# Kernel optimization log

Hardware: AMD Instinct MI355X
Metric: run time of the kernel (lower is better)

## Reference

```python
import jax, jax.numpy as jnp
import numpy as np

B, N, C = 32, 2248, 1024
D = 128            # bottleneck (down_size)
P = 200            # num_prompt_tokens
SCALE = D ** (-0.5)


def setup_inputs() -> dict:
    key = jax.random.key(0)
    k = jax.random.split(key, 5)
    return {
        "x": jax.random.normal(k[0], (B, N, C), dtype=jnp.float32),
        "W_down": jax.random.normal(k[1], (C, D), dtype=jnp.float32) * (C ** -0.5),
        "b_down": jax.random.normal(k[2], (D,), dtype=jnp.float32) * 0.01,
        "W_up": jax.random.normal(k[3], (D, C), dtype=jnp.float32) * (D ** -0.5),
        "b_up": jax.random.normal(k[4], (C,), dtype=jnp.float32) * 0.01,
        "gate": jnp.ones((), dtype=jnp.float32),
    }


def reference(x, W_down, b_down, W_up, b_up, gate):
    # down-projection + exact GELU (torch nn.GELU default is erf-based)
    down = jax.nn.gelu(jnp.einsum('bnc,cd->bnd', x, W_down) + b_down,
                       approximate=False)                      # [B, N, D]
    prompt_down = down[:, :P, :]                               # [B, P, D]
    token_down = down[:, P:, :]                                # [B, N-P, D]
    # prompt-token cross attention
    attn = jax.nn.softmax(
        jnp.einsum('bpd,btd->bpt', prompt_down, token_down) * SCALE, axis=-1)
    prompt_out = jnp.einsum('bpt,btd->bpd', attn, token_down)  # [B, P, D]
    combined = jnp.concatenate([prompt_out, token_down], axis=1)  # [B, N, D]
    up = jnp.einsum('bnd,dc->bnc', combined, W_up) + b_up      # [B, N, C]
    return gate * up
```

## Files before the change

kernel.cpp:

```cpp
#include <hip/hip_runtime.h>
#include <hip/hip_bf16.h>
#include <math.h>

#define B_   32
#define N_   2248
#define C_   1024
#define D_   128
#define P_   200
#define T_   2048
#define M_   (B_ * N_)
#define SCALE_ 0.08838834764831845f

typedef __bf16 bf16;
typedef __bf16 bf16x8 __attribute__((ext_vector_type(8)));
typedef __bf16 bf16x4 __attribute__((ext_vector_type(4)));
typedef float  f32x4  __attribute__((ext_vector_type(4)));
typedef unsigned int u32x4 __attribute__((ext_vector_type(4)));

#define VT_COL(dd, t) ((((((t) >> 3) ^ (((dd) >> 3) & 7)) << 3)) | ((t) & 7))

__device__ __forceinline__ void gl_lds16(const void* g, void* l) {
    __builtin_amdgcn_global_load_lds(
        (const __attribute__((address_space(1))) unsigned int*)g,
        (__attribute__((address_space(3))) unsigned int*)l,
        16, 0, 0);
}

__global__ void k_prep(const float* __restrict__ Wd, const float* __restrict__ Wu,
                       bf16* __restrict__ WtD, bf16* __restrict__ WtU) {
    int i = blockIdx.x * 256 + threadIdx.x;
    if (i >= 131072) return;
    int d = i >> 10, k = i & 1023;
    WtD[i] = (bf16)Wd[k * 128 + d];
    int c = i >> 7, e = i & 127;
    WtU[i] = (bf16)Wu[e * 1024 + c];
}

__launch_bounds__(256, 3)
__global__ void k_down(const float* __restrict__ x, const bf16* __restrict__ WtD,
                       const float* __restrict__ bd, bf16* __restrict__ down) {
    __shared__ __align__(16) char ring[3][16384];
    const int tid = threadIdx.x;
    const int lane = tid & 63, w = tid >> 6;
    const int wm = w >> 1, wn = w & 1;
    const int li = lane & 15, lg = lane >> 4;
    const int m0 = blockIdx.x * 64;

    const int cA0 = w * 2, cA1 = w * 2 + 1;
    const int ar0 = cA0 * 8 + (lane >> 3);
    const int ar1 = cA1 * 8 + (lane >> 3);
    const float* asrc0 = x + (size_t)(m0 + ar0) * C_ + ((((lane & 7) ^ (ar0 & 7)) * 16) >> 2);
    const float* asrc1 = x + (size_t)(m0 + ar1) * C_ + ((((lane & 7) ^ (ar1 & 7)) * 16) >> 2);
    const int br0 = cA0 * 16 + (lane >> 2);
    const int br1 = cA1 * 16 + (lane >> 2);
    const bf16* bsrc0 = WtD + (size_t)br0 * C_ + (((lane & 3) ^ (br0 & 3)) * 8);
    const bf16* bsrc1 = WtD + (size_t)br1 * C_ + (((lane & 3) ^ (br1 & 3)) * 8);

#define STAGE_(t_, s_) do {                                              \
        gl_lds16(asrc0 + (t_) * 32, ring[s_] + cA0 * 1024);              \
        gl_lds16(asrc1 + (t_) * 32, ring[s_] + cA1 * 1024);              \
        gl_lds16(bsrc0 + (t_) * 32, ring[s_] + 8192 + cA0 * 1024);       \
        gl_lds16(bsrc1 + (t_) * 32, ring[s_] + 8192 + cA1 * 1024);       \
    } while (0)

    f32x4 acc[2][4];
    const f32x4 zero = {0.f, 0.f, 0.f, 0.f};
#pragma unroll
    for (int i = 0; i < 2; i++)
#pragma unroll
        for (int j = 0; j < 4; j++) acc[i][j] = zero;

    STAGE_(0, 0);
    STAGE_(1, 1);

    for (int t = 0; t < 32; t++) {
        if (t < 31) { asm volatile("s_waitcnt vmcnt(4)" ::: "memory"); }
        else        { asm volatile("s_waitcnt vmcnt(0)" ::: "memory"); }
        __builtin_amdgcn_sched_barrier(0);
        __builtin_amdgcn_s_barrier();
        __builtin_amdgcn_sched_barrier(0);
        if (t + 2 < 32) {
            int s = (t + 2) % 3;
            STAGE_(t + 2, s);
        }
        const char* sa = ring[t % 3];
        const char* sb = sa + 8192;
        bf16x8 af[2];
#pragma unroll
        for (int f = 0; f < 2; f++) {
            int row = wm * 32 + f * 16 + li;
            const char* rb = sa + row * 128;
            int p0 = (2 * lg) ^ (row & 7), p1 = (2 * lg + 1) ^ (row & 7);
            f32x4 a0 = *(const f32x4*)(rb + p0 * 16);
            f32x4 a1 = *(const f32x4*)(rb + p1 * 16);
            bf16x8 o;
            o[0] = (bf16)a0[0]; o[1] = (bf16)a0[1]; o[2] = (bf16)a0[2]; o[3] = (bf16)a0[3];
            o[4] = (bf16)a1[0]; o[5] = (bf16)a1[1]; o[6] = (bf16)a1[2]; o[7] = (bf16)a1[3];
            af[f] = o;
        }
        bf16x8 bfr[4];
#pragma unroll
        for (int f = 0; f < 4; f++) {
            int row = wn * 64 + f * 16 + li;
            bfr[f] = *(const bf16x8*)(sb + row * 64 + ((lg ^ (row & 3)) * 16));
        }
#pragma unroll
        for (int fm = 0; fm < 2; fm++)
#pragma unroll
            for (int fn = 0; fn < 4; fn++)
                acc[fm][fn] = __builtin_amdgcn_mfma_f32_16x16x32_bf16(
                    af[fm], bfr[fn], acc[fm][fn], 0, 0, 0);
    }
#undef STAGE_

#pragma unroll
    for (int fn = 0; fn < 4; fn++) {
        int col = wn * 64 + fn * 16 + li;
        float bias = bd[col];
#pragma unroll
        for (int fm = 0; fm < 2; fm++) {
            int rb = m0 + wm * 32 + fm * 16 + lg * 4;
#pragma unroll
            for (int r = 0; r < 4; r++) {
                float v = acc[fm][fn][r] + bias;
                float g = 0.5f * v * (1.0f + erff(v * 0.70710678118654752f));
                down[(size_t)(rb + r) * D_ + col] = (bf16)g;
            }
        }
    }
}

__launch_bounds__(256, 3)
__global__ void k_fused(const bf16* __restrict__ down, bf16* __restrict__ pout,
                        const bf16* __restrict__ WtU, const float* __restrict__ bu,
                        const float* __restrict__ gate, float* __restrict__ out) {
    __shared__ bf16 Ks[64][136];
    __shared__ bf16 Vt[128][72];
    __shared__ bf16 Ps[4][16][72];
    const int tid = threadIdx.x;
    const int lane = tid & 63, w = tid >> 6;
    const int li = lane & 15, lg = lane >> 4;

    if (blockIdx.x < 128) {
        const int b  = blockIdx.x >> 2;
        const int qt = blockIdx.x & 3;
        const size_t base = (size_t)b * N_ * D_;

        bf16x8 qf[4];
#pragma unroll
        for (int kk = 0; kk < 4; kk++)
            qf[kk] = *(const bf16x8*)(down + base +
                        (size_t)(qt * 64 + w * 16 + li) * D_ + kk * 32 + lg * 8);

        float m_run[4], l_run[4];
        f32x4 acc[8];
        const f32x4 zero = {0.f, 0.f, 0.f, 0.f};
#pragma unroll
        for (int r = 0; r < 4; r++) { m_run[r] = -3.0e38f; l_run[r] = 0.f; }
#pragma unroll
        for (int fn = 0; fn < 8; fn++) acc[fn] = zero;

        for (int tt = 0; tt < 32; tt++) {
            __syncthreads();
#pragma unroll
            for (int it = 0; it < 4; it++) {
                int ch = tid + it * 256;
                int r = ch >> 4, c8 = (ch & 15) * 8;
                u32x4 v = *(const u32x4*)(down + base +
                              (size_t)(P_ + tt * 64 + r) * D_ + c8);
                *(u32x4*)&Ks[r][c8] = v;
                bf16 tmp[8];
                *(u32x4*)tmp = v;
#pragma unroll
                for (int j = 0; j < 8; j++) Vt[c8 + j][VT_COL(c8 + j, r)] = tmp[j];
            }
            __syncthreads();
            f32x4 s[4];
#pragma unroll
            for (int fn = 0; fn < 4; fn++) {
                s[fn] = zero;
#pragma unroll
                for (int kk = 0; kk < 4; kk++) {
                    bf16x8 kf = *(const bf16x8*)&Ks[fn * 16 + li][kk * 32 + lg * 8];
                    s[fn] = __builtin_amdgcn_mfma_f32_16x16x32_bf16(qf[kk], kf, s[fn], 0, 0, 0);
                }
                s[fn] *= SCALE_;
            }
#pragma unroll
            for (int r = 0; r < 4; r++) {
                float tmax = fmaxf(fmaxf(s[0][r], s[1][r]), fmaxf(s[2][r], s[3][r]));
#pragma unroll
                for (int off = 1; off < 16; off <<= 1)
                    tmax = fmaxf(tmax, __shfl_xor(tmax, off, 64));
                float mnew = fmaxf(m_run[r], tmax);
                float corr = __expf(m_run[r] - mnew);
                m_run[r] = mnew;
                float psum = 0.f;
#pragma unroll
                for (int fn = 0; fn < 4; fn++) {
                    float p = __expf(s[fn][r] - mnew);
                    psum += p;
                    Ps[w][lg * 4 + r][fn * 16 + li] = (bf16)p;
                }
#pragma unroll
                for (int off = 1; off < 16; off <<= 1)
                    psum += __shfl_xor(psum, off, 64);
                l_run[r] = l_run[r] * corr + psum;
#pragma unroll
                for (int fn = 0; fn < 8; fn++) acc[fn][r] *= corr;
            }
#pragma unroll
            for (int kk = 0; kk < 2; kk++) {
                bf16x8 pf = *(const bf16x8*)&Ps[w][li][kk * 32 + lg * 8];
#pragma unroll
                for (int fn = 0; fn < 8; fn++) {
                    int d = fn * 16 + li;
                    bf16x8 vf = *(const bf16x8*)&Vt[d][VT_COL(d, kk * 32 + lg * 8)];
                    acc[fn] = __builtin_amdgcn_mfma_f32_16x16x32_bf16(pf, vf, acc[fn], 0, 0, 0);
                }
            }
        }
#pragma unroll
        for (int r = 0; r < 4; r++) {
            int q = qt * 64 + w * 16 + lg * 4 + r;
            if (q < P_) {
                float inv = 1.0f / l_run[r];
#pragma unroll
                for (int fn = 0; fn < 8; fn++)
                    pout[(size_t)(b * P_ + q) * D_ + fn * 16 + li] = (bf16)(acc[fn][r] * inv);
            }
        }
    } else {
        const int wm = w >> 1, wn = w & 1;
        int bidu = blockIdx.x - 128;
        int wg = (bidu & 7) * 512 + (bidu >> 3);
        const int b  = wg >> 7;
        const int rt = (wg >> 3) & 15;
        const int nt = wg & 7;
        const size_t m0 = (size_t)b * N_ + P_ + rt * 128;
        const int n0 = nt * 128;

        const bf16* Bp = WtU + (size_t)(n0 + wn * 64 + li) * D_ + lg * 8;

        f32x4 acc[4][4];
        const f32x4 zero = {0.f, 0.f, 0.f, 0.f};
#pragma unroll
        for (int i = 0; i < 4; i++)
#pragma unroll
            for (int j = 0; j < 4; j++) acc[i][j] = zero;

#pragma unroll
        for (int kk = 0; kk < 4; kk++) {
            bf16x8 af[4], bf_[4];
#pragma unroll
            for (int f = 0; f < 4; f++) {
                af[f]  = *(const bf16x8*)(down + (m0 + wm * 64 + f * 16 + li) * D_ + kk * 32 + lg * 8);
                bf_[f] = *(const bf16x8*)(Bp + (size_t)(f * 16) * D_ + kk * 32);
            }
#pragma unroll
            for (int fm = 0; fm < 4; fm++)
#pragma unroll
                for (int fn = 0; fn < 4; fn++)
                    acc[fm][fn] = __builtin_amdgcn_mfma_f32_16x16x32_bf16(
                        af[fm], bf_[fn], acc[fm][fn], 0, 0, 0);
        }

        float g = gate[0];
#pragma unroll
        for (int fn = 0; fn < 4; fn++) {
            int c = n0 + wn * 64 + fn * 16 + li;
            float bias = bu[c];
#pragma unroll
            for (int fm = 0; fm < 4; fm++) {
                size_t rb = m0 + wm * 64 + fm * 16 + lg * 4;
#pragma unroll
                for (int r = 0; r < 4; r++)
                    out[(rb + r) * C_ + c] = g * (acc[fm][fn][r] + bias);
            }
        }
    }
}

__launch_bounds__(256, 3)
__global__ void k_up_prompt(const bf16* __restrict__ pout, const bf16* __restrict__ WtU,
                            const float* __restrict__ bu, const float* __restrict__ gate,
                            float* __restrict__ out) {
    const int tid = threadIdx.x;
    const int lane = tid & 63, wid = tid >> 6;
    const int wm = wid >> 1, wn = wid & 1;
    const int li = lane & 15, lg = lane >> 4;
    const int b  = blockIdx.x >> 4;
    const int pt = (blockIdx.x >> 3) & 1;
    const int nt = blockIdx.x & 7;
    const int n0 = nt * 128;

    const bf16* rp[4];
#pragma unroll
    for (int f = 0; f < 4; f++) {
        int n = pt * 128 + wm * 64 + f * 16 + li;
        int nc = n < P_ ? n : P_ - 1;
        rp[f] = pout + (size_t)(b * P_ + nc) * D_ + lg * 8;
    }
    const bf16* Bp = WtU + (size_t)(n0 + wn * 64 + li) * D_ + lg * 8;

    f32x4 acc[4][4];
    const f32x4 zero = {0.f, 0.f, 0.f, 0.f};
#pragma unroll
    for (int i = 0; i < 4; i++)
#pragma unroll
        for (int j = 0; j < 4; j++) acc[i][j] = zero;

#pragma unroll
    for (int kk = 0; kk < 4; kk++) {
        bf16x8 af[4], bf_[4];
#pragma unroll
        for (int f = 0; f < 4; f++) {
            af[f]  = *(const bf16x8*)(rp[f] + kk * 32);
            bf_[f] = *(const bf16x8*)(Bp + (size_t)(f * 16) * D_ + kk * 32);
        }
#pragma unroll
        for (int fm = 0; fm < 4; fm++)
#pragma unroll
            for (int fn = 0; fn < 4; fn++)
                acc[fm][fn] = __builtin_amdgcn_mfma_f32_16x16x32_bf16(
                    af[fm], bf_[fn], acc[fm][fn], 0, 0, 0);
    }

    float g = gate[0];
#pragma unroll
    for (int fn = 0; fn < 4; fn++) {
        int c = n0 + wn * 64 + fn * 16 + li;
        float bias = bu[c];
#pragma unroll
        for (int fm = 0; fm < 4; fm++) {
            int nr = pt * 128 + wm * 64 + fm * 16 + lg * 4;
#pragma unroll
            for (int r = 0; r < 4; r++) {
                if (nr + r < P_)
                    out[((size_t)b * N_ + nr + r) * C_ + c] = g * (acc[fm][fn][r] + bias);
            }
        }
    }
}

extern "C" void kernel_launch(void* const* d_in, const int* in_sizes, int n_in,
                              void* d_out, int out_size, void* d_ws, size_t ws_size,
                              hipStream_t stream) {
    const float* x    = (const float*)d_in[0];
    const float* Wd   = (const float*)d_in[1];
    const float* bd   = (const float*)d_in[2];
    const float* Wu   = (const float*)d_in[3];
    const float* bu   = (const float*)d_in[4];
    const float* gate = (const float*)d_in[5];
    float* out = (float*)d_out;

    char* w = (char*)d_ws;
    bf16* down = (bf16*)w;
    bf16* pout = (bf16*)(w + 18415616);
    bf16* WtD  = (bf16*)(w + 20054016);
    bf16* WtU  = (bf16*)(w + 20316160);

    k_prep<<<512, 256, 0, stream>>>(Wd, Wu, WtD, WtU);
    k_down<<<M_ / 64, 256, 0, stream>>>(x, WtD, bd, down);
    k_fused<<<128 + 4096, 256, 0, stream>>>(down, pout, WtU, bu, gate, out);
    k_up_prompt<<<512, 256, 0, stream>>>(pout, WtU, bu, gate, out);
}
```

Before: 271.1 us.

## Split prompt attention over four token chunks with a separate combine kernel

The attention part of the fused kernel moves from 128 blocks that each walk all 2048 tokens to 512 blocks that each handle a quarter of the tokens. Each block writes unnormalized partial outputs plus its running max and sum, and a new combine kernel merges them with log-sum-exp rescaling into the bf16 prompt output. The goal is to cut the long serial tail of the attention blocks, which otherwise run far longer than the up-projection tiles sharing the grid. The cost is an extra kernel launch and roughly 16 MB of fp32 partial-result traffic.

```diff
diff --git a/kernel.cpp b/kernel.cpp
--- a/kernel.cpp
+++ b/kernel.cpp
@@ -131,7 +131,8 @@
 }
 
 __launch_bounds__(256, 3)
-__global__ void k_fused(const bf16* __restrict__ down, bf16* __restrict__ pout,
+__global__ void k_fused(const bf16* __restrict__ down, float* __restrict__ Opart,
+                        float* __restrict__ Mpart, float* __restrict__ Lpart,
                         const bf16* __restrict__ WtU, const float* __restrict__ bu,
                         const float* __restrict__ gate, float* __restrict__ out) {
     __shared__ bf16 Ks[64][136];
@@ -141,10 +142,14 @@
     const int lane = tid & 63, w = tid >> 6;
     const int li = lane & 15, lg = lane >> 4;
 
-    if (blockIdx.x < 128) {
-        const int b  = blockIdx.x >> 2;
-        const int qt = blockIdx.x & 3;
+    if (blockIdx.x < 512) {
+        const int bid = blockIdx.x;
+        const int wg = (bid & 7) * 64 + (bid >> 3);
+        const int b  = wg >> 4;
+        const int qt = (wg >> 2) & 3;
+        const int th = wg & 3;
         const size_t base = (size_t)b * N_ * D_;
+        const int tbase = P_ + th * 512;
 
         bf16x8 qf[4];
 #pragma unroll
@@ -160,14 +165,14 @@
 #pragma unroll
         for (int fn = 0; fn < 8; fn++) acc[fn] = zero;
 
-        for (int tt = 0; tt < 32; tt++) {
+        for (int tt = 0; tt < 8; tt++) {
             __syncthreads();
 #pragma unroll
             for (int it = 0; it < 4; it++) {
                 int ch = tid + it * 256;
                 int r = ch >> 4, c8 = (ch & 15) * 8;
                 u32x4 v = *(const u32x4*)(down + base +
-                              (size_t)(P_ + tt * 64 + r) * D_ + c8);
+                              (size_t)(tbase + tt * 64 + r) * D_ + c8);
                 *(u32x4*)&Ks[r][c8] = v;
                 bf16 tmp[8];
                 *(u32x4*)tmp = v;
@@ -223,16 +228,18 @@
 #pragma unroll
         for (int r = 0; r < 4; r++) {
             int q = qt * 64 + w * 16 + lg * 4 + r;
-            if (q < P_) {
-                float inv = 1.0f / l_run[r];
-#pragma unroll
-                for (int fn = 0; fn < 8; fn++)
-                    pout[(size_t)(b * P_ + q) * D_ + fn * 16 + li] = (bf16)(acc[fn][r] * inv);
+            size_t ro = ((size_t)(b * 4 + th) * 256 + q) * 128;
+#pragma unroll
+            for (int fn = 0; fn < 8; fn++)
+                Opart[ro + fn * 16 + li] = acc[fn][r];
+            if (li == 0) {
+                Mpart[(b * 4 + th) * 256 + q] = m_run[r];
+                Lpart[(b * 4 + th) * 256 + q] = l_run[r];
             }
         }
     } else {
         const int wm = w >> 1, wn = w & 1;
-        int bidu = blockIdx.x - 128;
+        int bidu = blockIdx.x - 512;
         int wg = (bidu & 7) * 512 + (bidu >> 3);
         const int b  = wg >> 7;
         const int rt = (wg >> 3) & 15;
@@ -279,6 +286,40 @@
             }
         }
     }
+}
+
+__global__ void k_comb(const float* __restrict__ Opart, const float* __restrict__ Mpart,
+                       const float* __restrict__ Lpart, bf16* __restrict__ pout) {
+    int gid = blockIdx.x * 256 + threadIdx.x;
+    if (gid >= (B_ * P_ * D_) / 4) return;
+    int e = gid * 4;
+    int row = e >> 7;
+    int col = e & 127;
+    int b = row / P_;
+    int q = row - b * P_;
+    float mm[4], ll[4];
+    float m = -3.0e38f;
+#pragma unroll
+    for (int t = 0; t < 4; t++) {
+        mm[t] = Mpart[(b * 4 + t) * 256 + q];
+        ll[t] = Lpart[(b * 4 + t) * 256 + q];
+        m = fmaxf(m, mm[t]);
+    }
+    float a[4], lsum = 0.f;
+#pragma unroll
+    for (int t = 0; t < 4; t++) { a[t] = __expf(mm[t] - m); lsum += ll[t] * a[t]; }
+    float inv = 1.0f / lsum;
+    f32x4 o = {0.f, 0.f, 0.f, 0.f};
+#pragma unroll
+    for (int t = 0; t < 4; t++) {
+        f32x4 ot = *(const f32x4*)&Opart[((size_t)(b * 4 + t) * 256 + q) * 128 + col];
+#pragma unroll
+        for (int j = 0; j < 4; j++) o[j] += ot[j] * a[t];
+    }
+    bf16x4 ob;
+#pragma unroll
+    for (int j = 0; j < 4; j++) ob[j] = (bf16)(o[j] * inv);
+    *(bf16x4*)&pout[(size_t)row * 128 + col] = ob;
 }
 
 __launch_bounds__(256, 3)
@@ -355,13 +396,18 @@
     float* out = (float*)d_out;
 
     char* w = (char*)d_ws;
-    bf16* down = (bf16*)w;
-    bf16* pout = (bf16*)(w + 18415616);
-    bf16* WtD  = (bf16*)(w + 20054016);
-    bf16* WtU  = (bf16*)(w + 20316160);
+    bf16*  down  = (bf16*)w;
+    bf16*  pout  = (bf16*)(w + 18415616);
+    bf16*  WtD   = (bf16*)(w + 20054016);
+    bf16*  WtU   = (bf16*)(w + 20316160);
+    float* Opart = (float*)(w + 20578304);
+    float* Mpart = (float*)(w + 37355520);
+    float* Lpart = (float*)(w + 37486592);
 
     k_prep<<<512, 256, 0, stream>>>(Wd, Wu, WtD, WtU);
     k_down<<<M_ / 64, 256, 0, stream>>>(x, WtD, bd, down);
-    k_fused<<<128 + 4096, 256, 0, stream>>>(down, pout, WtU, bu, gate, out);
+    k_fused<<<512 + 4096, 256, 0, stream>>>(down, Opart, Mpart, Lpart,
+                                            WtU, bu, gate, out);
+    k_comb<<<800, 256, 0, stream>>>(Opart, Mpart, Lpart, pout);
     k_up_prompt<<<512, 256, 0, stream>>>(pout, WtU, bu, gate, out);
 }
```

After: 221.9 us. 18.1% less time.
